# Optimization experiments

Hardware: AMD Instinct MI355X
Metric: run time of the kernel (lower is better)

## Reference

```python
import jax, jax.numpy as jnp
import numpy as np

B, L, C, H = 4, 2048, 512, 8
D = C // H  # head_dim = 64


def _rope_tables(L, D):
    inv_freq = 1.0 / (10000.0 ** (np.arange(0, D, 2, dtype=np.float32) / D))
    t = np.arange(L, dtype=np.float32)
    freqs = np.outer(t, inv_freq)                      # (L, D/2)
    emb = np.concatenate([freqs, freqs], axis=-1)      # (L, D)
    return jnp.asarray(np.cos(emb)), jnp.asarray(np.sin(emb))


def setup_inputs() -> dict:
    key = jax.random.key(0)
    k1, k2, k3 = jax.random.split(key, 3)
    cos, sin = _rope_tables(L, D)
    return {
        "x": jax.random.normal(k1, (B, L, C), dtype=jnp.float32),
        "qkv_w": jax.random.normal(k2, (3 * C, C), dtype=jnp.float32) * 0.02,
        "qkv_b": jnp.zeros((3 * C,), dtype=jnp.float32),
        "proj_w": jax.random.normal(k3, (C, C), dtype=jnp.float32) * 0.02,
        "proj_b": jnp.zeros((C,), dtype=jnp.float32),
        "cos": cos,
        "sin": sin,
    }


def _rotate_half(x):
    x1, x2 = jnp.split(x, 2, axis=-1)
    return jnp.concatenate([-x2, x1], axis=-1)


def _apply_rope(x, cos, sin):
    # x: (B, H, L, D); cos/sin: (L, D)
    return x * cos[None, None] + _rotate_half(x) * sin[None, None]


def reference(x, qkv_w, qkv_b, proj_w, proj_b, cos, sin):
    b, l, c = x.shape
    scale = 1.0 / jnp.sqrt(jnp.float32(D))
    qkv = x @ qkv_w.T + qkv_b                          # (B, L, 3C)
    qkv = qkv.reshape(b, l, 3, H, D).transpose(2, 0, 3, 1, 4)  # (3, B, H, L, D)
    q, k, v = qkv[0], qkv[1], qkv[2]
    q = _apply_rope(q, cos, sin)
    k = _apply_rope(k, cos, sin)
    attn = jax.nn.softmax(scale * jnp.einsum('bhqd,bhkd->bhqk', q, k), axis=-1)
    out = jnp.einsum('bhqk,bhkd->bhqd', attn, v)       # (B, H, L, D)
    out = out.transpose(0, 2, 1, 3).reshape(b, l, c)   # (B, L, C)
    return out @ proj_w.T + proj_b
```

## Files before the change

### kernel.cpp

```cpp
#include <hip/hip_runtime.h>

#define CDIM 512
#define LDIM 2048
#define BDIM 4
#define HDIM 8
#define DDIM 64

typedef __attribute__((ext_vector_type(8))) short bf16x8;
typedef __attribute__((ext_vector_type(4))) float f32x4;
typedef __attribute__((ext_vector_type(2))) float f32x2;
typedef __attribute__((ext_vector_type(8))) unsigned short ushort8;

static __device__ __forceinline__ unsigned short f2bf(float f) {
  unsigned u = __float_as_uint(f);
  return (unsigned short)((u + 0x7FFFu + ((u >> 16) & 1u)) >> 16);
}

__global__ __launch_bounds__(256) void convert_kernel(
    const float* __restrict__ x, const float* __restrict__ qw,
    const float* __restrict__ pw, unsigned short* __restrict__ xb,
    unsigned short* __restrict__ wb, unsigned short* __restrict__ pwb) {
  const size_t i = ((size_t)blockIdx.x * 256 + threadIdx.x) * 8;
  const float* src; unsigned short* dst; size_t off;
  if (i < 4194304) { src = x;  dst = xb;  off = i; }
  else if (i < 4980736) { src = qw; dst = wb;  off = i - 4194304; }
  else { src = pw; dst = pwb; off = i - 4980736; }
  const float4 a = *(const float4*)(src + off);
  const float4 b = *(const float4*)(src + off + 4);
  ushort8 h;
  h[0] = f2bf(a.x); h[1] = f2bf(a.y); h[2] = f2bf(a.z); h[3] = f2bf(a.w);
  h[4] = f2bf(b.x); h[5] = f2bf(b.y); h[6] = f2bf(b.z); h[7] = f2bf(b.w);
  *(ushort8*)(dst + off) = h;
}

__global__ __launch_bounds__(256) void qkv_gemm_kernel(
    const unsigned short* __restrict__ xb, const unsigned short* __restrict__ wb,
    const float* __restrict__ bias, const float* __restrict__ cosT,
    const float* __restrict__ sinT, unsigned short* __restrict__ qb,
    unsigned short* __restrict__ kb, unsigned short* __restrict__ vt) {
  __shared__ char As[16384];
  __shared__ char Bs[16384];
  const int t  = threadIdx.x;
  const int w  = t >> 6, lane = t & 63;
  const int lo = lane & 15, hi = lane >> 4;
  const int wm = w >> 1, wn = w & 1;
  const int m0 = blockIdx.y * 128, n0 = blockIdx.x * 128;

  f32x4 acc[4][4];
  #pragma unroll
  for (int mt = 0; mt < 4; ++mt)
    #pragma unroll
    for (int nt = 0; nt < 4; ++nt) acc[mt][nt] = (f32x4){0.f, 0.f, 0.f, 0.f};

  const int srow   = t >> 3;
  const int schunk = ((t & 7) ^ (srow & 7)) << 4;
  const char* Ag = (const char*)xb;
  const char* Bg = (const char*)wb;

  for (int kt = 0; kt < CDIM; kt += 64) {
    #pragma unroll
    for (int s = 0; s < 4; ++s) {
      const int r = s * 32 + srow;
      __builtin_amdgcn_global_load_lds(
          (const __attribute__((address_space(1))) unsigned int*)
              (Ag + (size_t)(m0 + r) * 1024 + kt * 2 + schunk),
          (__attribute__((address_space(3))) unsigned int*)(As + s * 4096 + w * 1024),
          16, 0, 0);
      __builtin_amdgcn_global_load_lds(
          (const __attribute__((address_space(1))) unsigned int*)
              (Bg + (size_t)(n0 + r) * 1024 + kt * 2 + schunk),
          (__attribute__((address_space(3))) unsigned int*)(Bs + s * 4096 + w * 1024),
          16, 0, 0);
    }
    __syncthreads();
    #pragma unroll
    for (int ks = 0; ks < 2; ++ks) {
      bf16x8 af[4], bfr[4];
      #pragma unroll
      for (int mt = 0; mt < 4; ++mt)
        af[mt] = *(const bf16x8*)(As + (wm * 64 + mt * 16 + lo) * 128
                                  + (((ks * 4 + hi) ^ (lo & 7)) << 4));
      #pragma unroll
      for (int nt = 0; nt < 4; ++nt)
        bfr[nt] = *(const bf16x8*)(Bs + (wn * 64 + nt * 16 + lo) * 128
                                   + (((ks * 4 + hi) ^ (lo & 7)) << 4));
      #pragma unroll
      for (int mt = 0; mt < 4; ++mt)
        #pragma unroll
        for (int nt = 0; nt < 4; ++nt)
          acc[mt][nt] = __builtin_amdgcn_mfma_f32_16x16x32_bf16(
              af[mt], bfr[nt], acc[mt][nt], 0, 0, 0);
    }
    __syncthreads();
  }

  const int nbase = n0 + wn * 64;
  const int typ   = nbase >> 9;
  const int hh    = (nbase >> 6) & 7;
  const int bb    = m0 >> 11;
  const int lbase = (m0 & 2047) + wm * 64;

  float bq[4];
  #pragma unroll
  for (int nt = 0; nt < 4; ++nt) bq[nt] = bias[nbase + nt * 16 + lo];
  #pragma unroll
  for (int mt = 0; mt < 4; ++mt)
    #pragma unroll
    for (int nt = 0; nt < 4; ++nt)
      #pragma unroll
      for (int reg = 0; reg < 4; ++reg) acc[mt][nt][reg] += bq[nt];

  if (typ == 2) {
    unsigned short* vbase = vt + (size_t)(bb * HDIM + hh) * DDIM * LDIM;
    #pragma unroll
    for (int mt = 0; mt < 4; ++mt)
      #pragma unroll
      for (int nt = 0; nt < 4; ++nt) {
        const int d = nt * 16 + lo;
        #pragma unroll
        for (int reg = 0; reg < 4; ++reg) {
          const int l = lbase + mt * 16 + hi * 4 + reg;
          vbase[(size_t)d * LDIM + l] = f2bf(acc[mt][nt][reg]);
        }
      }
  } else {
    unsigned short* dstb = (typ ? kb : qb) + (size_t)(bb * HDIM + hh) * LDIM * DDIM;
    #pragma unroll
    for (int mt = 0; mt < 4; ++mt)
      #pragma unroll
      for (int nt = 0; nt < 4; ++nt) {
        const int d   = nt * 16 + lo;
        const float sgn = (nt & 2) ? 1.f : -1.f;
        #pragma unroll
        for (int reg = 0; reg < 4; ++reg) {
          const int l = lbase + mt * 16 + hi * 4 + reg;
          const float c = cosT[l * 64 + d], s = sinT[l * 64 + d];
          const float v = acc[mt][nt][reg] * c + sgn * acc[mt][nt ^ 2][reg] * s;
          dstb[(size_t)l * DDIM + d] = f2bf(v);
        }
      }
  }
}

#define CLOG2 0.18033688f

__global__ __launch_bounds__(512, 4) void attn_kernel(
    unsigned short* __restrict__ qb, const unsigned short* __restrict__ kb,
    const unsigned short* __restrict__ vt) {
  __shared__ char Lds[65536];
  const int t    = threadIdx.x;
  const int w    = t >> 6, lane = t & 63;
  const int lo   = lane & 15, hi = lane >> 4;
  const int wq   = w & 3, half = w >> 2;
  const int bh   = blockIdx.y;
  const int q0   = blockIdx.x * 128 + wq * 32;
  const int kb0  = half * 1024;

  const char* Kb = (const char*)kb + (size_t)bh * (LDIM * DDIM * 2);
  const char* Vb = (const char*)vt + (size_t)bh * (LDIM * DDIM * 2);
  unsigned short* Qb = qb + (size_t)bh * (LDIM * DDIM);

  bf16x8 qf[2][2];
  #pragma unroll
  for (int g = 0; g < 2; ++g)
    #pragma unroll
    for (int kd = 0; kd < 2; ++kd)
      qf[g][kd] = *(const bf16x8*)((const char*)(Qb + (size_t)(q0 + g * 16 + lo) * DDIM)
                                   + kd * 64 + hi * 16);

  f32x4 o[2][4];
  float mrun[2] = {0.f, 0.f}, mc[2] = {0.f, 0.f}, lpart[2] = {0.f, 0.f};
  #pragma unroll
  for (int g = 0; g < 2; ++g)
    #pragma unroll
    for (int r = 0; r < 4; ++r) o[g][r] = (f32x4){0.f, 0.f, 0.f, 0.f};

  const int krow = wq * 8 + (lane >> 3);
  const int kch  = ((lane & 7) ^ (krow & 7)) << 4;
  const int vrow = wq * 16 + (lane >> 2);
  const int vch  = ((lane & 3) ^ ((vrow >> 1) & 3)) << 4;

  auto stage = [&](int tile, int buf) {
    __builtin_amdgcn_global_load_lds(
        (const __attribute__((address_space(1))) unsigned int*)
            (Kb + (size_t)(kb0 + tile * 32 + krow) * 128 + kch),
        (__attribute__((address_space(3))) unsigned int*)
            (Lds + (half * 2 + buf) * 4096 + wq * 1024),
        16, 0, 0);
    __builtin_amdgcn_global_load_lds(
        (const __attribute__((address_space(1))) unsigned int*)
            (Vb + (size_t)vrow * (LDIM * 2) + (size_t)(kb0 + tile * 32) * 2 + vch),
        (__attribute__((address_space(3))) unsigned int*)
            (Lds + 16384 + (half * 2 + buf) * 4096 + wq * 1024),
        16, 0, 0);
  };

  stage(0, 0);

  char* Pwb = Lds + 32768 + w * 4096;

  for (int kt = 0; kt < 32; ++kt) {
    const int cur = kt & 1;
    const int nk  = kt < 31 ? kt + 1 : 31;
    stage(nk, cur ^ 1);
    asm volatile("s_waitcnt vmcnt(2)");
    __builtin_amdgcn_s_barrier();
    __builtin_amdgcn_sched_barrier(0);

    const char* Kl = Lds + (half * 2 + cur) * 4096;
    const char* Vl = Lds + 16384 + (half * 2 + cur) * 4096;

    f32x4 sv[2][2];
    __builtin_amdgcn_s_setprio(1);
    #pragma unroll
    for (int nt = 0; nt < 2; ++nt) {
      sv[0][nt] = (f32x4){0.f, 0.f, 0.f, 0.f};
      sv[1][nt] = (f32x4){0.f, 0.f, 0.f, 0.f};
      const int key = nt * 16 + lo;
      #pragma unroll
      for (int kd = 0; kd < 2; ++kd) {
        const bf16x8 kf = *(const bf16x8*)(Kl + key * 128
                            + (((kd * 4 + hi) ^ (lo & 7)) << 4));
        sv[0][nt] = __builtin_amdgcn_mfma_f32_16x16x32_bf16(kf, qf[0][kd], sv[0][nt], 0, 0, 0);
        sv[1][nt] = __builtin_amdgcn_mfma_f32_16x16x32_bf16(kf, qf[1][kd], sv[1][nt], 0, 0, 0);
      }
    }
    __builtin_amdgcn_s_setprio(0);

    #pragma unroll
    for (int g = 0; g < 2; ++g) {
      const float* sflat = (const float*)sv[g];
      const f32x2 cc2 = {CLOG2, CLOG2};
      const f32x2 mm2 = {-mc[g], -mc[g]};
      float pv[8];
      float ps = 0.f;
      #pragma unroll
      for (int i = 0; i < 4; ++i) {
        f32x2 a; a[0] = sflat[2*i]; a[1] = sflat[2*i+1];
        f32x2 xr;
        asm("v_pk_fma_f32 %0, %1, %2, %3" : "=v"(xr) : "v"(a), "v"(cc2), "v"(mm2));
        float p0, p1;
        asm("v_exp_f32 %0, %1" : "=v"(p0) : "v"(xr[0]));
        asm("v_exp_f32 %0, %1" : "=v"(p1) : "v"(xr[1]));
        pv[2*i] = p0; pv[2*i+1] = p1;
        ps += p0; ps += p1;
      }

      if (__builtin_expect((bool)__ballot(ps > 65536.f), 0)) {
        float mx = -1e30f;
        #pragma unroll
        for (int i = 0; i < 8; ++i) mx = fmaxf(mx, sflat[i]);
        mx = fmaxf(mx, __shfl_xor(mx, 16));
        mx = fmaxf(mx, __shfl_xor(mx, 32));
        const float newm = fmaxf(mrun[g], mx);
        const float al   = exp2f((mrun[g] - newm) * CLOG2);
        lpart[g] *= al;
        #pragma unroll
        for (int r = 0; r < 4; ++r) {
          const float aq = __shfl(al, (hi << 2) + r);
          #pragma unroll
          for (int dt = 0; dt < 4; ++dt) o[g][dt][r] *= aq;
        }
        mrun[g] = newm;
        mc[g]   = newm * CLOG2;
        ps = 0.f;
        #pragma unroll
        for (int i = 0; i < 8; ++i) {
          const float p = exp2f(fmaf(sflat[i], CLOG2, -mc[g]));
          pv[i] = p;
          ps += p;
        }
      }
      lpart[g] += ps;

      #pragma unroll
      for (int nt = 0; nt < 2; ++nt) {
        unsigned w0, w1;
        asm("v_cvt_pk_bf16_f32 %0, %1, %2"
            : "=v"(w0) : "v"(pv[nt*4+0]), "v"(pv[nt*4+1]));
        asm("v_cvt_pk_bf16_f32 %0, %1, %2"
            : "=v"(w1) : "v"(pv[nt*4+2]), "v"(pv[nt*4+3]));
        uint2 d2; d2.x = w0; d2.y = w1;
        *(uint2*)(Pwb + g * 2048 + lo * 128
                  + ((nt * 32 + hi * 8) ^ ((lo & 7) << 4))) = d2;
      }
    }

    __builtin_amdgcn_s_setprio(1);
    {
      const bf16x8 pf0 = *(const bf16x8*)(Pwb + lo * 128
                           + ((hi ^ (lo & 7)) << 4));
      const bf16x8 pf1 = *(const bf16x8*)(Pwb + 2048 + lo * 128
                           + ((hi ^ (lo & 7)) << 4));
      #pragma unroll
      for (int dt = 0; dt < 4; ++dt) {
        const int d = dt * 16 + lo;
        const bf16x8 vf = *(const bf16x8*)(Vl + d * 64
                            + ((hi ^ ((d >> 1) & 3)) << 4));
        o[0][dt] = __builtin_amdgcn_mfma_f32_16x16x32_bf16(pf0, vf, o[0][dt], 0, 0, 0);
        o[1][dt] = __builtin_amdgcn_mfma_f32_16x16x32_bf16(pf1, vf, o[1][dt], 0, 0, 0);
      }
    }
    __builtin_amdgcn_s_setprio(0);

    __builtin_amdgcn_sched_barrier(0);
    __builtin_amdgcn_s_barrier();
  }

  asm volatile("s_waitcnt vmcnt(0)");
  __syncthreads();

  float rs[2];
  #pragma unroll
  for (int g = 0; g < 2; ++g) {
    rs[g] = lpart[g];
    rs[g] += __shfl_xor(rs[g], 16);
    rs[g] += __shfl_xor(rs[g], 32);
  }

  if (half == 1) {
    #pragma unroll
    for (int g = 0; g < 2; ++g) {
      #pragma unroll
      for (int dt = 0; dt < 4; ++dt)
        #pragma unroll
        for (int r = 0; r < 4; ++r)
          *(float*)(Lds + wq * 8192
                    + ((g * 16 + hi * 4 + r) * 64 + dt * 16 + lo) * 4) = o[g][dt][r];
      if (hi == 0) {
        *(float*)(Lds + 32768 + wq * 256 + g * 64 + lo * 4)       = rs[g];
        *(float*)(Lds + 32768 + wq * 256 + 128 + g * 64 + lo * 4) = mrun[g];
      }
    }
  }
  __syncthreads();
  if (half == 0) {
    #pragma unroll
    for (int g = 0; g < 2; ++g)
      #pragma unroll
      for (int r = 0; r < 4; ++r) {
        const int qrow = hi * 4 + r;
        const float m_a = __shfl(mrun[g], qrow);
        const float l_a = __shfl(rs[g], qrow);
        const float l_b = *(const float*)(Lds + 32768 + wq * 256 + g * 64 + qrow * 4);
        const float m_b = *(const float*)(Lds + 32768 + wq * 256 + 128 + g * 64 + qrow * 4);
        const float m  = fmaxf(m_a, m_b);
        const float aa = exp2f((m_a - m) * CLOG2);
        const float ab = exp2f((m_b - m) * CLOG2);
        const float inv = 1.f / (l_a * aa + l_b * ab);
        const int q = q0 + g * 16 + qrow;
        #pragma unroll
        for (int dt = 0; dt < 4; ++dt) {
          const float ob = *(const float*)(Lds + wq * 8192
                            + ((g * 16 + qrow) * 64 + dt * 16 + lo) * 4);
          Qb[(size_t)q * DDIM + dt * 16 + lo] =
              f2bf((o[g][dt][r] * aa + ob * ab) * inv);
        }
      }
  }
}

__global__ __launch_bounds__(256) void proj_gemm_kernel(
    const unsigned short* __restrict__ ab, const unsigned short* __restrict__ pwb,
    const float* __restrict__ bias, float* __restrict__ out) {
  __shared__ char As[8192];
  __shared__ char Bs[16384];
  const int t  = threadIdx.x;
  const int w  = t >> 6, lane = t & 63;
  const int lo = lane & 15, hi = lane >> 4;
  const int wm = w >> 1, wn = w & 1;
  const int m0 = blockIdx.y * 64, n0 = blockIdx.x * 128;

  f32x4 acc[2][4];
  #pragma unroll
  for (int mt = 0; mt < 2; ++mt)
    #pragma unroll
    for (int nt = 0; nt < 4; ++nt) acc[mt][nt] = (f32x4){0.f, 0.f, 0.f, 0.f};

  const int srow   = t >> 3;
  const int schunk = ((t & 7) ^ (srow & 7)) << 4;
  const char* Ag = (const char*)ab;
  const char* Bg = (const char*)pwb;

  for (int kt = 0; kt < CDIM; kt += 64) {
    const int hh = kt >> 6;
    #pragma unroll
    for (int s = 0; s < 2; ++s) {
      const int r = s * 32 + srow;
      const int m = m0 + r;
      const int bb = m >> 11, l = m & 2047;
      __builtin_amdgcn_global_load_lds(
          (const __attribute__((address_space(1))) unsigned int*)
              (Ag + ((size_t)(bb * HDIM + hh) * LDIM + l) * 128 + schunk),
          (__attribute__((address_space(3))) unsigned int*)(As + s * 4096 + w * 1024),
          16, 0, 0);
    }
    #pragma unroll
    for (int s = 0; s < 4; ++s) {
      const int r = s * 32 + srow;
      __builtin_amdgcn_global_load_lds(
          (const __attribute__((address_space(1))) unsigned int*)
              (Bg + (size_t)(n0 + r) * 1024 + kt * 2 + schunk),
          (__attribute__((address_space(3))) unsigned int*)(Bs + s * 4096 + w * 1024),
          16, 0, 0);
    }
    __syncthreads();
    #pragma unroll
    for (int ks = 0; ks < 2; ++ks) {
      bf16x8 af[2], bfr[4];
      #pragma unroll
      for (int mt = 0; mt < 2; ++mt)
        af[mt] = *(const bf16x8*)(As + (wm * 32 + mt * 16 + lo) * 128
                                  + (((ks * 4 + hi) ^ (lo & 7)) << 4));
      #pragma unroll
      for (int nt = 0; nt < 4; ++nt)
        bfr[nt] = *(const bf16x8*)(Bs + (wn * 64 + nt * 16 + lo) * 128
                                   + (((ks * 4 + hi) ^ (lo & 7)) << 4));
      #pragma unroll
      for (int mt = 0; mt < 2; ++mt)
        #pragma unroll
        for (int nt = 0; nt < 4; ++nt)
          acc[mt][nt] = __builtin_amdgcn_mfma_f32_16x16x32_bf16(
              af[mt], bfr[nt], acc[mt][nt], 0, 0, 0);
    }
    __syncthreads();
  }

  const int nn = n0 + wn * 64;
  float bp[4];
  #pragma unroll
  for (int nt = 0; nt < 4; ++nt) bp[nt] = bias[nn + nt * 16 + lo];
  #pragma unroll
  for (int mt = 0; mt < 2; ++mt)
    #pragma unroll
    for (int nt = 0; nt < 4; ++nt)
      #pragma unroll
      for (int reg = 0; reg < 4; ++reg) {
        const int m = m0 + wm * 32 + mt * 16 + hi * 4 + reg;
        out[(size_t)m * CDIM + nn + nt * 16 + lo] = acc[mt][nt][reg] + bp[nt];
      }
}

extern "C" void kernel_launch(void* const* d_in, const int* in_sizes, int n_in,
                              void* d_out, int out_size, void* d_ws, size_t ws_size,
                              hipStream_t stream) {
  const float* x      = (const float*)d_in[0];
  const float* qkv_w  = (const float*)d_in[1];
  const float* qkv_b  = (const float*)d_in[2];
  const float* proj_w = (const float*)d_in[3];
  const float* proj_b = (const float*)d_in[4];
  const float* cosT   = (const float*)d_in[5];
  const float* sinT   = (const float*)d_in[6];
  float* out = (float*)d_out;

  unsigned short* qb  = (unsigned short*)d_ws;
  unsigned short* kb  = qb + (size_t)BDIM * HDIM * LDIM * DDIM;
  unsigned short* vt  = kb + (size_t)BDIM * HDIM * LDIM * DDIM;
  unsigned short* xb  = vt + (size_t)BDIM * HDIM * LDIM * DDIM;
  unsigned short* wb  = xb + (size_t)BDIM * LDIM * CDIM;
  unsigned short* pwb = wb + (size_t)3 * CDIM * CDIM;

  convert_kernel<<<dim3(2560), 256, 0, stream>>>(x, qkv_w, proj_w, xb, wb, pwb);
  qkv_gemm_kernel<<<dim3(12, 64), 256, 0, stream>>>(xb, wb, qkv_b, cosT, sinT,
                                                    qb, kb, vt);
  attn_kernel<<<dim3(16, 32), 512, 0, stream>>>(qb, kb, vt);
  proj_gemm_kernel<<<dim3(4, 128), 256, 0, stream>>>(qb, pwb, proj_b, out);
}
```

Baseline: 97.28 us.

## Keep P in registers for PV MFMA, double key tile, XCD-aware block mapping

The attention kernel now processes 64-key tiles instead of 32, halving the number of barrier-synchronised iterations. Softmax probabilities stay in registers and feed a 16x16x16 bf16 MFMA directly with transposed operands, which removes the LDS round trip for P. All three GEMM and attention kernels switch to a flat grid with XCD-aware block remapping so blocks sharing data land on the same XCD's L2. The epilogue is rewritten for vectorised stores in the new accumulator layout. The costs are more LDS per block, more registers, and smaller-K MFMAs.

```diff
diff --git a/kernel.cpp b/kernel.cpp
--- a/kernel.cpp
+++ b/kernel.cpp
@@ -7,6 +7,7 @@
 #define DDIM 64
 
 typedef __attribute__((ext_vector_type(8))) short bf16x8;
+typedef __attribute__((ext_vector_type(4))) short bf16x4;
 typedef __attribute__((ext_vector_type(4))) float f32x4;
 typedef __attribute__((ext_vector_type(2))) float f32x2;
 typedef __attribute__((ext_vector_type(8))) unsigned short ushort8;
@@ -44,7 +45,10 @@
   const int w  = t >> 6, lane = t & 63;
   const int lo = lane & 15, hi = lane >> 4;
   const int wm = w >> 1, wn = w & 1;
-  const int m0 = blockIdx.y * 128, n0 = blockIdx.x * 128;
+  const int flat = blockIdx.x;
+  const int xcd = flat & 7, j = flat >> 3;
+  const int m0 = (xcd + 8 * (j / 12)) * 128;
+  const int n0 = (j % 12) * 128;
 
   f32x4 acc[4][4];
   #pragma unroll
@@ -152,8 +156,10 @@
   const int w    = t >> 6, lane = t & 63;
   const int lo   = lane & 15, hi = lane >> 4;
   const int wq   = w & 3, half = w >> 2;
-  const int bh   = blockIdx.y;
-  const int q0   = blockIdx.x * 128 + wq * 32;
+  const int flat = blockIdx.x;
+  const int xcd  = flat & 7, jj = flat >> 3;
+  const int bh   = xcd + 8 * (jj >> 4);
+  const int q0   = (jj & 15) * 128 + wq * 32;
   const int kb0  = half * 1024;
 
   const char* Kb = (const char*)kb + (size_t)bh * (LDIM * DDIM * 2);
@@ -175,45 +181,46 @@
     #pragma unroll
     for (int r = 0; r < 4; ++r) o[g][r] = (f32x4){0.f, 0.f, 0.f, 0.f};
 
-  const int krow = wq * 8 + (lane >> 3);
-  const int kch  = ((lane & 7) ^ (krow & 7)) << 4;
-  const int vrow = wq * 16 + (lane >> 2);
-  const int vch  = ((lane & 3) ^ ((vrow >> 1) & 3)) << 4;
-
+  const int sl0  = lane;
   auto stage = [&](int tile, int buf) {
-    __builtin_amdgcn_global_load_lds(
-        (const __attribute__((address_space(1))) unsigned int*)
-            (Kb + (size_t)(kb0 + tile * 32 + krow) * 128 + kch),
-        (__attribute__((address_space(3))) unsigned int*)
-            (Lds + (half * 2 + buf) * 4096 + wq * 1024),
-        16, 0, 0);
-    __builtin_amdgcn_global_load_lds(
-        (const __attribute__((address_space(1))) unsigned int*)
-            (Vb + (size_t)vrow * (LDIM * 2) + (size_t)(kb0 + tile * 32) * 2 + vch),
-        (__attribute__((address_space(3))) unsigned int*)
-            (Lds + 16384 + (half * 2 + buf) * 4096 + wq * 1024),
-        16, 0, 0);
+    #pragma unroll
+    for (int s = 0; s < 2; ++s) {
+      const int slot = s * 64 + sl0;
+      const int rl = slot >> 3, c = slot & 7;
+      const int sw16 = ((c ^ (rl & 7)) << 4);
+      __builtin_amdgcn_global_load_lds(
+          (const __attribute__((address_space(1))) unsigned int*)
+              (Kb + (size_t)(kb0 + tile * 64 + wq * 16 + rl) * 128 + sw16),
+          (__attribute__((address_space(3))) unsigned int*)
+              (Lds + (half * 2 + buf) * 8192 + wq * 2048 + slot * 16),
+          16, 0, 0);
+      __builtin_amdgcn_global_load_lds(
+          (const __attribute__((address_space(1))) unsigned int*)
+              (Vb + (size_t)(wq * 16 + rl) * (LDIM * 2)
+                  + (size_t)(kb0 + tile * 64) * 2 + sw16),
+          (__attribute__((address_space(3))) unsigned int*)
+              (Lds + 32768 + (half * 2 + buf) * 8192 + wq * 2048 + slot * 16),
+          16, 0, 0);
+    }
   };
 
   stage(0, 0);
 
-  char* Pwb = Lds + 32768 + w * 4096;
-
-  for (int kt = 0; kt < 32; ++kt) {
+  for (int kt = 0; kt < 16; ++kt) {
     const int cur = kt & 1;
-    const int nk  = kt < 31 ? kt + 1 : 31;
+    const int nk  = kt < 15 ? kt + 1 : 15;
     stage(nk, cur ^ 1);
-    asm volatile("s_waitcnt vmcnt(2)");
+    asm volatile("s_waitcnt vmcnt(4)");
     __builtin_amdgcn_s_barrier();
     __builtin_amdgcn_sched_barrier(0);
 
-    const char* Kl = Lds + (half * 2 + cur) * 4096;
-    const char* Vl = Lds + 16384 + (half * 2 + cur) * 4096;
-
-    f32x4 sv[2][2];
+    const char* Kl = Lds + (half * 2 + cur) * 8192;
+    const char* Vl = Lds + 32768 + (half * 2 + cur) * 8192;
+
+    f32x4 sv[2][4];
     __builtin_amdgcn_s_setprio(1);
     #pragma unroll
-    for (int nt = 0; nt < 2; ++nt) {
+    for (int nt = 0; nt < 4; ++nt) {
       sv[0][nt] = (f32x4){0.f, 0.f, 0.f, 0.f};
       sv[1][nt] = (f32x4){0.f, 0.f, 0.f, 0.f};
       const int key = nt * 16 + lo;
@@ -227,46 +234,48 @@
     }
     __builtin_amdgcn_s_setprio(0);
 
+    bf16x4 paf[2][4];
     #pragma unroll
     for (int g = 0; g < 2; ++g) {
-      const float* sflat = (const float*)sv[g];
       const f32x2 cc2 = {CLOG2, CLOG2};
       const f32x2 mm2 = {-mc[g], -mc[g]};
-      float pv[8];
       float ps = 0.f;
-      #pragma unroll
-      for (int i = 0; i < 4; ++i) {
-        f32x2 a; a[0] = sflat[2*i]; a[1] = sflat[2*i+1];
-        f32x2 xr;
-        asm("v_pk_fma_f32 %0, %1, %2, %3" : "=v"(xr) : "v"(a), "v"(cc2), "v"(mm2));
-        float p0, p1;
-        asm("v_exp_f32 %0, %1" : "=v"(p0) : "v"(xr[0]));
-        asm("v_exp_f32 %0, %1" : "=v"(p1) : "v"(xr[1]));
-        pv[2*i] = p0; pv[2*i+1] = p1;
-        ps += p0; ps += p1;
+      float pv[16];
+      #pragma unroll
+      for (int nt = 0; nt < 4; ++nt) {
+        f32x2 a0, a1, x0, x1;
+        a0[0] = sv[g][nt][0]; a0[1] = sv[g][nt][1];
+        a1[0] = sv[g][nt][2]; a1[1] = sv[g][nt][3];
+        asm("v_pk_fma_f32 %0, %1, %2, %3" : "=v"(x0) : "v"(a0), "v"(cc2), "v"(mm2));
+        asm("v_pk_fma_f32 %0, %1, %2, %3" : "=v"(x1) : "v"(a1), "v"(cc2), "v"(mm2));
+        float p0, p1, p2, p3;
+        asm("v_exp_f32 %0, %1" : "=v"(p0) : "v"(x0[0]));
+        asm("v_exp_f32 %0, %1" : "=v"(p1) : "v"(x0[1]));
+        asm("v_exp_f32 %0, %1" : "=v"(p2) : "v"(x1[0]));
+        asm("v_exp_f32 %0, %1" : "=v"(p3) : "v"(x1[1]));
+        pv[nt*4+0] = p0; pv[nt*4+1] = p1; pv[nt*4+2] = p2; pv[nt*4+3] = p3;
+        ps += p0 + p1 + p2 + p3;
       }
 
       if (__builtin_expect((bool)__ballot(ps > 65536.f), 0)) {
         float mx = -1e30f;
         #pragma unroll
-        for (int i = 0; i < 8; ++i) mx = fmaxf(mx, sflat[i]);
+        for (int i = 0; i < 16; ++i) mx = fmaxf(mx, ((const float*)sv[g])[i]);
         mx = fmaxf(mx, __shfl_xor(mx, 16));
         mx = fmaxf(mx, __shfl_xor(mx, 32));
         const float newm = fmaxf(mrun[g], mx);
         const float al   = exp2f((mrun[g] - newm) * CLOG2);
         lpart[g] *= al;
         #pragma unroll
-        for (int r = 0; r < 4; ++r) {
-          const float aq = __shfl(al, (hi << 2) + r);
+        for (int dt = 0; dt < 4; ++dt)
           #pragma unroll
-          for (int dt = 0; dt < 4; ++dt) o[g][dt][r] *= aq;
-        }
+          for (int r = 0; r < 4; ++r) o[g][dt][r] *= al;
         mrun[g] = newm;
         mc[g]   = newm * CLOG2;
         ps = 0.f;
         #pragma unroll
-        for (int i = 0; i < 8; ++i) {
-          const float p = exp2f(fmaf(sflat[i], CLOG2, -mc[g]));
+        for (int i = 0; i < 16; ++i) {
+          const float p = exp2f(fmaf(((const float*)sv[g])[i], CLOG2, -mc[g]));
           pv[i] = p;
           ps += p;
         }
@@ -274,31 +283,28 @@
       lpart[g] += ps;
 
       #pragma unroll
-      for (int nt = 0; nt < 2; ++nt) {
-        unsigned w0, w1;
+      for (int nt = 0; nt < 4; ++nt) {
+        unsigned u0, u1;
         asm("v_cvt_pk_bf16_f32 %0, %1, %2"
-            : "=v"(w0) : "v"(pv[nt*4+0]), "v"(pv[nt*4+1]));
+            : "=v"(u0) : "v"(pv[nt*4+0]), "v"(pv[nt*4+1]));
         asm("v_cvt_pk_bf16_f32 %0, %1, %2"
-            : "=v"(w1) : "v"(pv[nt*4+2]), "v"(pv[nt*4+3]));
-        uint2 d2; d2.x = w0; d2.y = w1;
-        *(uint2*)(Pwb + g * 2048 + lo * 128
-                  + ((nt * 32 + hi * 8) ^ ((lo & 7) << 4))) = d2;
+            : "=v"(u1) : "v"(pv[nt*4+2]), "v"(pv[nt*4+3]));
+        uint2 d2; d2.x = u0; d2.y = u1;
+        paf[g][nt] = *(const bf16x4*)&d2;
       }
     }
 
     __builtin_amdgcn_s_setprio(1);
-    {
-      const bf16x8 pf0 = *(const bf16x8*)(Pwb + lo * 128
-                           + ((hi ^ (lo & 7)) << 4));
-      const bf16x8 pf1 = *(const bf16x8*)(Pwb + 2048 + lo * 128
-                           + ((hi ^ (lo & 7)) << 4));
+    #pragma unroll
+    for (int nt = 0; nt < 4; ++nt) {
       #pragma unroll
       for (int dt = 0; dt < 4; ++dt) {
         const int d = dt * 16 + lo;
-        const bf16x8 vf = *(const bf16x8*)(Vl + d * 64
-                            + ((hi ^ ((d >> 1) & 3)) << 4));
-        o[0][dt] = __builtin_amdgcn_mfma_f32_16x16x32_bf16(pf0, vf, o[0][dt], 0, 0, 0);
-        o[1][dt] = __builtin_amdgcn_mfma_f32_16x16x32_bf16(pf1, vf, o[1][dt], 0, 0, 0);
+        const bf16x4 vf = *(const bf16x4*)(Vl + d * 128
+                            + (((nt * 2 + (hi >> 1)) ^ (lo & 7)) << 4)
+                            + (hi & 1) * 8);
+        o[0][dt] = __builtin_amdgcn_mfma_f32_16x16x16bf16_1k(vf, paf[0][nt], o[0][dt], 0, 0, 0);
+        o[1][dt] = __builtin_amdgcn_mfma_f32_16x16x16bf16_1k(vf, paf[1][nt], o[1][dt], 0, 0, 0);
       }
     }
     __builtin_amdgcn_s_setprio(0);
@@ -310,12 +316,12 @@
   asm volatile("s_waitcnt vmcnt(0)");
   __syncthreads();
 
-  float rs[2];
+  float rsum[2];
   #pragma unroll
   for (int g = 0; g < 2; ++g) {
-    rs[g] = lpart[g];
-    rs[g] += __shfl_xor(rs[g], 16);
-    rs[g] += __shfl_xor(rs[g], 32);
+    rsum[g] = lpart[g];
+    rsum[g] += __shfl_xor(rsum[g], 16);
+    rsum[g] += __shfl_xor(rsum[g], 32);
   }
 
   if (half == 1) {
@@ -323,40 +329,40 @@
     for (int g = 0; g < 2; ++g) {
       #pragma unroll
       for (int dt = 0; dt < 4; ++dt)
-        #pragma unroll
-        for (int r = 0; r < 4; ++r)
-          *(float*)(Lds + wq * 8192
-                    + ((g * 16 + hi * 4 + r) * 64 + dt * 16 + lo) * 4) = o[g][dt][r];
+        *(f32x4*)(Lds + wq * 8192
+                  + ((g * 16 + lo) * 64 + dt * 16 + hi * 4) * 4) = o[g][dt];
       if (hi == 0) {
-        *(float*)(Lds + 32768 + wq * 256 + g * 64 + lo * 4)       = rs[g];
-        *(float*)(Lds + 32768 + wq * 256 + 128 + g * 64 + lo * 4) = mrun[g];
+        *(float*)(Lds + 32768 + wq * 512 + (g * 16 + lo) * 4)       = rsum[g];
+        *(float*)(Lds + 32768 + wq * 512 + 128 + (g * 16 + lo) * 4) = mrun[g];
       }
     }
   }
   __syncthreads();
   if (half == 0) {
     #pragma unroll
-    for (int g = 0; g < 2; ++g)
-      #pragma unroll
-      for (int r = 0; r < 4; ++r) {
-        const int qrow = hi * 4 + r;
-        const float m_a = __shfl(mrun[g], qrow);
-        const float l_a = __shfl(rs[g], qrow);
-        const float l_b = *(const float*)(Lds + 32768 + wq * 256 + g * 64 + qrow * 4);
-        const float m_b = *(const float*)(Lds + 32768 + wq * 256 + 128 + g * 64 + qrow * 4);
-        const float m  = fmaxf(m_a, m_b);
-        const float aa = exp2f((m_a - m) * CLOG2);
-        const float ab = exp2f((m_b - m) * CLOG2);
-        const float inv = 1.f / (l_a * aa + l_b * ab);
-        const int q = q0 + g * 16 + qrow;
-        #pragma unroll
-        for (int dt = 0; dt < 4; ++dt) {
-          const float ob = *(const float*)(Lds + wq * 8192
-                            + ((g * 16 + qrow) * 64 + dt * 16 + lo) * 4);
-          Qb[(size_t)q * DDIM + dt * 16 + lo] =
-              f2bf((o[g][dt][r] * aa + ob * ab) * inv);
-        }
-      }
+    for (int g = 0; g < 2; ++g) {
+      const float l_b = *(const float*)(Lds + 32768 + wq * 512 + (g * 16 + lo) * 4);
+      const float m_b = *(const float*)(Lds + 32768 + wq * 512 + 128 + (g * 16 + lo) * 4);
+      const float m  = fmaxf(mrun[g], m_b);
+      const float aa = exp2f((mrun[g] - m) * CLOG2);
+      const float ab = exp2f((m_b - m) * CLOG2);
+      const float inv = 1.f / (rsum[g] * aa + l_b * ab);
+      const int q = q0 + g * 16 + lo;
+      #pragma unroll
+      for (int dt = 0; dt < 4; ++dt) {
+        const f32x4 ob = *(const f32x4*)(Lds + wq * 8192
+                          + ((g * 16 + lo) * 64 + dt * 16 + hi * 4) * 4);
+        const float r0 = (o[g][dt][0] * aa + ob[0] * ab) * inv;
+        const float r1 = (o[g][dt][1] * aa + ob[1] * ab) * inv;
+        const float r2 = (o[g][dt][2] * aa + ob[2] * ab) * inv;
+        const float r3 = (o[g][dt][3] * aa + ob[3] * ab) * inv;
+        unsigned u0, u1;
+        asm("v_cvt_pk_bf16_f32 %0, %1, %2" : "=v"(u0) : "v"(r0), "v"(r1));
+        asm("v_cvt_pk_bf16_f32 %0, %1, %2" : "=v"(u1) : "v"(r2), "v"(r3));
+        uint2 d2; d2.x = u0; d2.y = u1;
+        *(uint2*)((char*)Qb + (size_t)q * 128 + dt * 32 + hi * 8) = d2;
+      }
+    }
   }
 }
 
@@ -369,7 +375,10 @@
   const int w  = t >> 6, lane = t & 63;
   const int lo = lane & 15, hi = lane >> 4;
   const int wm = w >> 1, wn = w & 1;
-  const int m0 = blockIdx.y * 64, n0 = blockIdx.x * 128;
+  const int flat = blockIdx.x;
+  const int xcd = flat & 7, j = flat >> 3;
+  const int m0 = (xcd + 8 * (j >> 2)) * 64;
+  const int n0 = (j & 3) * 128;
 
   f32x4 acc[2][4];
   #pragma unroll
@@ -461,8 +470,8 @@
   unsigned short* pwb = wb + (size_t)3 * CDIM * CDIM;
 
   convert_kernel<<<dim3(2560), 256, 0, stream>>>(x, qkv_w, proj_w, xb, wb, pwb);
-  qkv_gemm_kernel<<<dim3(12, 64), 256, 0, stream>>>(xb, wb, qkv_b, cosT, sinT,
-                                                    qb, kb, vt);
-  attn_kernel<<<dim3(16, 32), 512, 0, stream>>>(qb, kb, vt);
-  proj_gemm_kernel<<<dim3(4, 128), 256, 0, stream>>>(qb, pwb, proj_b, out);
-}
+  qkv_gemm_kernel<<<dim3(768), 256, 0, stream>>>(xb, wb, qkv_b, cosT, sinT,
+                                                 qb, kb, vt);
+  attn_kernel<<<dim3(512), 512, 0, stream>>>(qb, kb, vt);
+  proj_gemm_kernel<<<dim3(512), 256, 0, stream>>>(qb, pwb, proj_b, out);
+}
```

Result: slower. 107.4 us (+10.4%).
